# Performance work log

Hardware: AMD Instinct MI355X
Metric: run time of the kernel (lower is better)

Reference implementation:

```python
import jax, jax.numpy as jnp
import numpy as np

N_HEADS = 16
NOPE = 128
ROPE = 64
VDIM = 128
HEAD_DIM = NOPE + ROPE  # 192


def apply_rope(x, cos, sin):
    # x: [B, S, H, D] with D even; pairs (a, b) rotated by complex freqs.
    B, S, H, D = x.shape
    xr = x.reshape(B, S, H, D // 2, 2)
    a, b = xr[..., 0], xr[..., 1]
    c = cos[None, :, None, :]
    s = sin[None, :, None, :]
    out = jnp.stack([a * c - b * s, a * s + b * c], axis=-1)
    return out.reshape(B, S, H, D)


def setup_inputs() -> dict:
    key = jax.random.key(0)
    ks = jax.random.split(key, 8)
    B, S, DIM = 1, 2048, 2048
    x = jax.random.normal(ks[0], (B, S, DIM), dtype=jnp.float32)
    wq = jax.random.normal(ks[1], (N_HEADS * HEAD_DIM, DIM), dtype=jnp.float32) * (DIM ** -0.5)
    wk = jax.random.normal(ks[2], (N_HEADS * HEAD_DIM, DIM), dtype=jnp.float32) * (DIM ** -0.5)
    wv = jax.random.normal(ks[3], (N_HEADS * VDIM, DIM), dtype=jnp.float32) * (DIM ** -0.5)
    wo = jax.random.normal(ks[4], (DIM, N_HEADS * VDIM), dtype=jnp.float32) * ((N_HEADS * VDIM) ** -0.5)
    # rotary freqs: theta = 10000^{-2i/d}, angles = pos * theta
    inv_freq = 1.0 / (10000.0 ** (np.arange(0, ROPE, 2, dtype=np.float32) / ROPE))
    angles = np.arange(S, dtype=np.float32)[:, None] * inv_freq[None, :]  # [S, 32]
    freqs_cos = jnp.asarray(np.cos(angles))
    freqs_sin = jnp.asarray(np.sin(angles))
    # additive causal mask
    mask = jnp.where(jnp.triu(jnp.ones((S, S), dtype=bool), k=1), -1e9, 0.0).astype(jnp.float32)
    return {"x": x, "wq": wq, "wk": wk, "wv": wv, "wo": wo,
            "freqs_cos": freqs_cos, "freqs_sin": freqs_sin, "mask": mask, "start_pos": 0}


def reference(x, wq, wk, wv, wo, freqs_cos, freqs_sin, mask, start_pos):
    B, S, DIM = x.shape
    q = (x @ wq.T).reshape(B, S, N_HEADS, HEAD_DIM)
    k = (x @ wk.T).reshape(B, S, N_HEADS, HEAD_DIM)
    v = (x @ wv.T).reshape(B, S, N_HEADS, VDIM)
    q_nope, q_pe = q[..., :NOPE], q[..., NOPE:]
    k_nope, k_pe = k[..., :NOPE], k[..., NOPE:]
    q_pe = apply_rope(q_pe, freqs_cos, freqs_sin)
    k_pe = apply_rope(k_pe, freqs_cos, freqs_sin)
    scores = (jnp.einsum('bshd,bthd->bsht', q_nope, k_nope)
              + jnp.einsum('bshd,bthd->bsht', q_pe, k_pe)) * (HEAD_DIM ** -0.5)
    scores = scores + mask[None, :, None, :]
    probs = jax.nn.softmax(scores.astype(jnp.float32), axis=-1).astype(x.dtype)
    out = jnp.einsum('bsht,bthd->bshd', probs, v)
    return out.reshape(B, S, N_HEADS * VDIM) @ wo.T
```

## Files before the change

### kernel.cpp

```cpp
#include <hip/hip_runtime.h>
#include <hip/hip_bf16.h>
#include <math.h>

#define NH 16
#define NOPE 128
#define ROPE 64
#define VDIM 128
#define HD 192
#define SEQ 2048
#define DIM 2048
#define QKD (NH * HD)
#define VD  (NH * VDIM)
#define QKVS 8192

typedef __attribute__((ext_vector_type(8))) short short8;
typedef __attribute__((ext_vector_type(4))) short short4v;
typedef __attribute__((ext_vector_type(4))) float f32x4;
typedef unsigned int u32;

#define WAIT_VM8  0x0F78
#define WAIT_VM6  0x0F76
#define WAIT_VM4  0x0F74
#define WAIT_VM0  0x0F70
#define WAIT_LGKM 0xC07F

static __device__ inline short f2bf(float f) {
  union { float f; unsigned u; } v; v.f = f;
  unsigned r = (v.u + 0x7fffu + ((v.u >> 16) & 1u)) >> 16;
  return (short)r;
}
static __device__ inline float bf2f(unsigned short u) {
  union { unsigned u; float f; } v; v.u = ((unsigned)u) << 16;
  return v.f;
}

static __device__ __forceinline__ void gload16(const short* g, short* l) {
  __builtin_amdgcn_global_load_lds(
      (const __attribute__((address_space(1))) u32*)g,
      (__attribute__((address_space(3))) u32*)l, 16, 0, 0);
}


#define LSA(pp) (Lsm + (pp) * 65536)
#define LSB(pp) (Lsm + (pp) * 65536 + 32768)

#define RDA(pp, kh, mh) do { \
  const char* p_ = LSA(pp) + abase + (mh) * 8192 + ((kh) ? cx1 : cx0); \
  afr[(mh) * 4 + 0] = *(const short8*)(p_ + 0); \
  afr[(mh) * 4 + 1] = *(const short8*)(p_ + 2048); \
  afr[(mh) * 4 + 2] = *(const short8*)(p_ + 4096); \
  afr[(mh) * 4 + 3] = *(const short8*)(p_ + 6144); \
} while (0)

#define RDB(pp, kh) do { \
  const char* p_ = LSB(pp) + bbase + ((kh) ? cx1 : cx0); \
  bfr[0] = *(const short8*)(p_ + 0); \
  bfr[1] = *(const short8*)(p_ + 2048); \
  bfr[2] = *(const short8*)(p_ + 4096); \
  bfr[3] = *(const short8*)(p_ + 6144); \
} while (0)

#define SGA(kt, c) gload16(srcA[c] + (kt) * 64, (short*)(LSA((kt) & 1) + ((c) * 512 + tid) * 16))
#define SGB(kt, c) gload16(srcB[c] + (kt) * 64, (short*)(LSB((kt) & 1) + ((c) * 512 + tid) * 16))
#define G1S(kt) do { SGA(kt, 0); SGA(kt, 2); SGB(kt, 0); SGB(kt, 1); } while (0)
#define G2S(kt) do { SGA(kt, 1); SGA(kt, 3); SGB(kt, 2); SGB(kt, 3); } while (0)

#define MFMA1(mi, ni) \
  acc[mi][ni] = __builtin_amdgcn_mfma_f32_16x16x32_bf16(afr[mi], bfr[ni], acc[mi][ni], 0, 0, 0)

#define MM(mh) do { \
  MFMA1((mh)*4+0, 0); MFMA1((mh)*4+1, 0); MFMA1((mh)*4+2, 0); MFMA1((mh)*4+3, 0); \
  MFMA1((mh)*4+0, 1); MFMA1((mh)*4+1, 1); MFMA1((mh)*4+2, 1); MFMA1((mh)*4+3, 1); \
  MFMA1((mh)*4+0, 2); MFMA1((mh)*4+1, 2); MFMA1((mh)*4+2, 2); MFMA1((mh)*4+3, 2); \
  MFMA1((mh)*4+0, 3); MFMA1((mh)*4+1, 3); MFMA1((mh)*4+2, 3); MFMA1((mh)*4+3, 3); \
} while (0)

#define GBAR() __builtin_amdgcn_s_barrier()
#define GLGKM0() __builtin_amdgcn_s_waitcnt(WAIT_LGKM)
#define GPRIO1() __builtin_amdgcn_s_setprio(1)
#define GPRIO0() __builtin_amdgcn_s_setprio(0)
#define GNOP ((void)0)

#define TILE(pp, SP1, SP4, VMW) do { \
  RDA(pp, 0, 0); RDB(pp, 0); SP1; \
  GBAR(); GLGKM0(); GPRIO1(); MM(0); GPRIO0(); GBAR(); \
  RDA(pp, 0, 1); \
  GBAR(); GLGKM0(); GPRIO1(); MM(1); GPRIO0(); GBAR(); \
  RDA(pp, 1, 0); RDB(pp, 1); \
  GBAR(); GLGKM0(); GPRIO1(); MM(0); GPRIO0(); GBAR(); \
  RDA(pp, 1, 1); SP4; \
  GBAR(); GLGKM0(); GPRIO1(); MM(1); GPRIO0(); VMW; GBAR(); \
} while (0)

__global__ __launch_bounds__(512, 2) void gemm256_bt(
    const short* __restrict__ A, const short* __restrict__ B,
    short* __restrict__ C, int K, int lda, int ldb, int ldc) {
  __shared__ __align__(16) char Lsm[131072];

  const int tid = threadIdx.x;
  const int lane = tid & 63;
  const int l15 = lane & 15;
  const int quad = lane >> 4;
  const int wv = tid >> 6;
  const int wr = wv >> 2, wc = wv & 3;

  const int bid = blockIdx.x;
  const int xcd = bid & 7;
  const int idx = bid >> 3;
  const int m0 = (idx & 7) * 256;
  const int n0 = (xcd * 4 + (idx >> 3)) * 256;

  const int trow = tid >> 3;
  const int scol = ((tid & 7) * 8) ^ ((trow & 7) * 8);
  const short* srcA[4]; const short* srcB[4];
#pragma unroll
  for (int c = 0; c < 4; ++c) {
    srcA[c] = A + (size_t)(m0 + c * 64 + trow) * lda + scol;
    srcB[c] = B + (size_t)(n0 + c * 64 + trow) * ldb + scol;
  }

  const int abase = (wr * 128 + l15) * 128;
  const int bbase = (wc * 64 + l15) * 128;
  const int cx0 = (quad * 16) ^ ((l15 & 7) * 16);
  const int cx1 = (64 + quad * 16) ^ ((l15 & 7) * 16);

  f32x4 acc[8][4];
#pragma unroll
  for (int i = 0; i < 8; ++i)
#pragma unroll
    for (int j = 0; j < 4; ++j) acc[i][j] = (f32x4)(0.f);
  short8 afr[8], bfr[4];

  const int NT = K >> 6;

  G1S(0); G2S(0); G1S(1);
  __builtin_amdgcn_s_waitcnt(WAIT_VM4);
  GBAR();

  int kt = 0;
  for (; kt + 4 <= NT; kt += 2) {
    TILE(0, G2S(kt + 1), G1S(kt + 2), __builtin_amdgcn_s_waitcnt(WAIT_VM4));
    TILE(1, G2S(kt + 2), G1S(kt + 3), __builtin_amdgcn_s_waitcnt(WAIT_VM4));
  }
  TILE(0, G2S(kt + 1), GNOP, __builtin_amdgcn_s_waitcnt(WAIT_VM0));
  TILE(1, GNOP, GNOP, GNOP);

#pragma unroll
  for (int m = 0; m < 8; ++m) {
    const size_t rb = (size_t)(m0 + wr * 128 + m * 16 + quad * 4) * ldc +
                      n0 + wc * 64 + l15;
#pragma unroll
    for (int n = 0; n < 4; ++n)
#pragma unroll
      for (int r = 0; r < 4; ++r)
        C[rb + (size_t)r * ldc + n * 16] = f2bf(acc[m][n][r]);
  }
}

template <bool BF16OUT>
__global__ __launch_bounds__(256) void gemm_bt(
    const short* __restrict__ A, const short* __restrict__ B,
    void* __restrict__ Cv, int K, int lda, int ldb, int ldc, float oscale) {
  __shared__ __align__(16) short Ls[4][2][4096];

  const int tid = threadIdx.x;
  const int lane = tid & 63;
  const int wave = tid >> 6;
  const int wr = wave >> 1, wc = wave & 1;
  const int lane15 = lane & 15, quad = lane >> 4;
  const int m0 = blockIdx.y * 128, n0 = blockIdx.x * 128;

  const short* gA[4]; const short* gB[4];
#pragma unroll
  for (int i = 0; i < 4; ++i) {
    int gidx = i * 64 + lane;
    int r = gidx >> 2, p = gidx & 3;
    int g = (p ^ ((r >> 1) & 3)) * 8;
    gA[i] = A + (size_t)(m0 + wr * 64 + r) * lda + g;
    gB[i] = B + (size_t)(n0 + wc * 64 + r) * ldb + g;
  }

  f32x4 acc[4][4];
#pragma unroll
  for (int i = 0; i < 4; ++i)
#pragma unroll
    for (int j = 0; j < 4; ++j) acc[i][j] = (f32x4)(0.f);

#pragma unroll
  for (int i = 0; i < 4; ++i) gload16(gA[i], &Ls[wave][0][i * 512]);
#pragma unroll
  for (int i = 0; i < 4; ++i) gload16(gB[i], &Ls[wave][0][2048 + i * 512]);

  const int rsw = (lane15 >> 1) & 3;
  for (int k0 = 0; k0 < K; k0 += 32) {
    const int cur = (k0 >> 5) & 1;
    __builtin_amdgcn_s_waitcnt(WAIT_LGKM);
    if (k0 + 32 < K) {
      const int nxt = cur ^ 1;
#pragma unroll
      for (int i = 0; i < 4; ++i) gload16(gA[i] + k0 + 32, &Ls[wave][nxt][i * 512]);
#pragma unroll
      for (int i = 0; i < 4; ++i) gload16(gB[i] + k0 + 32, &Ls[wave][nxt][2048 + i * 512]);
      __builtin_amdgcn_s_waitcnt(WAIT_VM8);
    } else {
      __builtin_amdgcn_s_waitcnt(WAIT_VM0);
    }
    const short* bufp = &Ls[wave][cur][0];
    short8 af[4], bfv[4];
#pragma unroll
    for (int i = 0; i < 4; ++i)
      af[i] = *(const short8*)&bufp[(i * 16 + lane15) * 32 + (quad ^ rsw) * 8];
#pragma unroll
    for (int j = 0; j < 4; ++j)
      bfv[j] = *(const short8*)&bufp[2048 + (j * 16 + lane15) * 32 + (quad ^ rsw) * 8];
#pragma unroll
    for (int i = 0; i < 4; ++i)
#pragma unroll
      for (int j = 0; j < 4; ++j)
        acc[i][j] = __builtin_amdgcn_mfma_f32_16x16x32_bf16(af[i], bfv[j], acc[i][j], 0, 0, 0);
  }

#pragma unroll
  for (int i = 0; i < 4; ++i)
#pragma unroll
    for (int j = 0; j < 4; ++j)
#pragma unroll
      for (int r = 0; r < 4; ++r) {
        size_t idx = (size_t)(m0 + wr * 64 + i * 16 + quad * 4 + r) * ldc +
                     n0 + wc * 64 + j * 16 + lane15;
        if (BF16OUT)
          ((short*)Cv)[idx] = f2bf(acc[i][j][r] * oscale);
        else
          ((float*)Cv)[idx] = acc[i][j][r];
      }
}

__global__ __launch_bounds__(256) void rope_qk(
    short* __restrict__ qk, const float* __restrict__ cosf, const float* __restrict__ sinf) {
  int idx = blockIdx.x * blockDim.x + threadIdx.x;
  int j = idx & 31;
  int h = (idx >> 5) & (NH - 1);
  int s = idx >> 9;
  if (s >= SEQ) return;

  float c = cosf[s * 32 + j];
  float sn = sinf[s * 32 + j];
  size_t rowb = (size_t)s * QKVS + h * HD + NOPE + 2 * j;

  u32* pq = (u32*)(qk + rowb);
  u32 w = *pq;
  float a = bf2f((unsigned short)(w & 0xffff));
  float b = bf2f((unsigned short)(w >> 16));
  *pq = (u32)(unsigned short)f2bf(a * c - b * sn) |
        ((u32)(unsigned short)f2bf(a * sn + b * c) << 16);

  u32* pk = (u32*)(qk + rowb + QKD);
  w = *pk;
  a = bf2f((unsigned short)(w & 0xffff));
  b = bf2f((unsigned short)(w >> 16));
  *pk = (u32)(unsigned short)f2bf(a * c - b * sn) |
        ((u32)(unsigned short)f2bf(a * sn + b * c) << 16);
}

__global__ __launch_bounds__(256) void bf16_convert(
    const float* __restrict__ in, short* __restrict__ out, int n4) {
  int i = blockIdx.x * 256 + threadIdx.x;
  if (i >= n4) return;
  float4 f = ((const float4*)in)[i];
  short4v o;
  o.x = f2bf(f.x); o.y = f2bf(f.y); o.z = f2bf(f.z); o.w = f2bf(f.w);
  ((short4v*)out)[i] = o;
}

__global__ __launch_bounds__(256) void conv_wqkv(
    const float* __restrict__ wq, const float* __restrict__ wk,
    const float* __restrict__ wv, short* __restrict__ wqkv, int n4) {
  int i = blockIdx.x * 256 + threadIdx.x;
  if (i >= n4) return;
  int row = i >> 9;
  float4 f;
  if (row < QKD) f = ((const float4*)wq)[i];
  else if (row < 2 * QKD) f = ((const float4*)wk)[i - QKD * (DIM / 4)];
  else f = ((const float4*)wv)[i - 2 * QKD * (DIM / 4)];
  short4v o;
  o.x = f2bf(f.x); o.y = f2bf(f.y); o.z = f2bf(f.z); o.w = f2bf(f.w);
  ((short4v*)wqkv)[i] = o;
}

__global__ __launch_bounds__(256) void vt_bf16(
    const short* __restrict__ vb, short* __restrict__ vtb) {
  __shared__ short tile[64][74];
  const int t0 = blockIdx.x * 64;
  const int c0 = blockIdx.y * 64;
  const int tid = threadIdx.x;
#pragma unroll
  for (int i = 0; i < 16; ++i) {
    int idx = i * 256 + tid;
    int r = idx >> 6, c = idx & 63;
    tile[r][c] = vb[(size_t)(t0 + r) * QKVS + c0 + c];
  }
  __syncthreads();
  const int h = c0 >> 7;
  const int dbase = c0 & 127;
#pragma unroll
  for (int i = 0; i < 16; ++i) {
    int idx = i * 256 + tid;
    int d = idx >> 6, t = idx & 63;
    vtb[(size_t)h * VDIM * SEQ + (size_t)(dbase + d) * SEQ + t0 + t] = tile[t][d];
  }
}

#define BQ 128
#define BT 64
#define CHT 8
#define PSTR 76
#define MFIX 8.0f

__global__ __launch_bounds__(512, 4) void attn_part(
    const short* __restrict__ qk,
    const short* __restrict__ vtb,
    short* __restrict__ Opart,
    float* __restrict__ lpart)
{
  __shared__ __align__(16) short Ks[BT * 192];
  __shared__ __align__(16) short Vt[VDIM * BT];
  __shared__ __align__(16) short Ps[8 * 16 * PSTR];

  const int xcd = blockIdx.x;
  const int i0 = blockIdx.y;
  const int h = xcd + ((i0 >= 40) ? 8 : 0);
  int jj = (i0 >= 40) ? (i0 - 40) : i0;
  int qtb = 15;
  while (jj >= (qtb >> 2) + 1) { jj -= (qtb >> 2) + 1; --qtb; }
  const int chk = jj;

  const int tid = threadIdx.x;
  const int wave = tid >> 6;
  const int lane = tid & 63;
  const int lane15 = lane & 15;
  const int quad = lane >> 4;
  const int g = qtb >> 2;
  const int slot = h * 40 + (g + 1) * (2 * g + (qtb & 3)) + chk;
  const int R0 = qtb * BQ;
  const int NT = 2 * qtb + 2;
  const int kt_beg = chk * CHT;
  const int kt_end = min(kt_beg + CHT, NT);
  const float scale = 0.072168784f;

  const int qrow = R0 + wave * 16 + lane15;
  short8 qf[6];
  const short* qbase = qk + (size_t)qrow * QKVS + h * HD + quad * 8;
#pragma unroll
  for (int kc = 0; kc < 6; ++kc) qf[kc] = *(const short8*)(qbase + kc * 32);

  const short* kb = qk + QKD;
  int lKoff[3]; const short* gK[3];
#pragma unroll
  for (int i = 0; i < 3; ++i) {
    int id = i * 512 + tid;
    int row = id / 24, cX = id - row * 24;
    int ch = cX ^ (row & 7);
    lKoff[i] = id * 8;
    gK[i] = kb + (size_t)row * QKVS + h * HD + ch * 8;
  }
  const short* gV[2]; short* lV[2];
#pragma unroll
  for (int i = 0; i < 2; ++i) {
    int id = i * 512 + tid;
    int row = id >> 3, cX = id & 7;
    int ch = cX ^ (row & 7);
    lV[i] = &Vt[id * 8];
    gV[i] = vtb + (size_t)h * VDIM * SEQ + (size_t)row * SEQ + ch * 8;
  }

  f32x4 oacc[8];
#pragma unroll
  for (int i = 0; i < 8; ++i) oacc[i] = (f32x4)(0.f);
  float lsum[4] = {0.f, 0.f, 0.f, 0.f};

  short* pw = &Ps[wave * 16 * PSTR];

  for (int kt = kt_beg; kt < kt_end; ++kt) {
    const int t0 = kt * BT;
    __syncthreads();
#pragma unroll
    for (int i = 0; i < 3; ++i) gload16(gK[i] + (size_t)t0 * QKVS, &Ks[lKoff[i]]);
#pragma unroll
    for (int i = 0; i < 2; ++i) gload16(gV[i] + t0, lV[i]);
    __syncthreads();

    f32x4 sacc[4];
    __builtin_amdgcn_s_setprio(1);
#pragma unroll
    for (int c = 0; c < 4; ++c) {
      sacc[c] = (f32x4)(0.f);
      const int row = c * 16 + lane15;
#pragma unroll
      for (int kc = 0; kc < 6; ++kc) {
        int cX = (4 * kc + quad) ^ (lane15 & 7);
        short8 kf = *(const short8*)&Ks[row * 192 + cX * 8];
        sacc[c] = __builtin_amdgcn_mfma_f32_16x16x32_bf16(qf[kc], kf, sacc[c], 0, 0, 0);
      }
    }
    __builtin_amdgcn_s_setprio(0);

    if (kt >= 2 * qtb) {
#pragma unroll
      for (int c = 0; c < 4; ++c)
#pragma unroll
        for (int r = 0; r < 4; ++r) {
          int tg = t0 + c * 16 + lane15;
          int qg = R0 + wave * 16 + quad * 4 + r;
          if (tg > qg) sacc[c][r] = -1e30f;
        }
    }

#pragma unroll
    for (int c = 0; c < 4; ++c)
#pragma unroll
      for (int r = 0; r < 4; ++r) {
        float p = __expf(sacc[c][r] * scale - MFIX);
        lsum[r] += p;
        pw[(quad * 4 + r) * PSTR + c * 16 + lane15] = f2bf(p);
      }

    short8 pf0 = *(const short8*)&pw[lane15 * PSTR + quad * 8];
    short8 pf1 = *(const short8*)&pw[lane15 * PSTR + 32 + quad * 8];
    __builtin_amdgcn_s_setprio(1);
#pragma unroll
    for (int ch = 0; ch < 8; ++ch) {
      const int row = ch * 16 + lane15;
      int cX0 = quad ^ (lane15 & 7);
      int cX1 = (4 + quad) ^ (lane15 & 7);
      short8 vf0 = *(const short8*)&Vt[row * 64 + cX0 * 8];
      short8 vf1 = *(const short8*)&Vt[row * 64 + cX1 * 8];
      oacc[ch] = __builtin_amdgcn_mfma_f32_16x16x32_bf16(pf0, vf0, oacc[ch], 0, 0, 0);
      oacc[ch] = __builtin_amdgcn_mfma_f32_16x16x32_bf16(pf1, vf1, oacc[ch], 0, 0, 0);
    }
    __builtin_amdgcn_s_setprio(0);
  }

  short* op = Opart + (size_t)slot * (128 * 128);
#pragma unroll
  for (int ch = 0; ch < 8; ++ch)
#pragma unroll
    for (int r = 0; r < 4; ++r)
      op[(wave * 16 + quad * 4 + r) * 128 + ch * 16 + lane15] = f2bf(oacc[ch][r]);

  float red[4];
#pragma unroll
  for (int r = 0; r < 4; ++r) {
    float s = lsum[r];
    s += __shfl_xor(s, 1, 64);
    s += __shfl_xor(s, 2, 64);
    s += __shfl_xor(s, 4, 64);
    s += __shfl_xor(s, 8, 64);
    red[r] = s;
  }
  if (lane15 == 0) {
#pragma unroll
    for (int r = 0; r < 4; ++r)
      lpart[(size_t)slot * 128 + wave * 16 + quad * 4 + r] = red[r];
  }
}

__global__ __launch_bounds__(256) void attn_combine(
    const short* __restrict__ Opart, const float* __restrict__ lpart,
    short* __restrict__ aob) {
  const int qt64 = blockIdx.x, h = blockIdx.y;
  const int qtb = qt64 >> 1;
  const int half = qt64 & 1;
  const int g = qtb >> 2;
  const int nact = g + 1;
  const int base = h * 40 + (g + 1) * (2 * g + (qtb & 3));
  const int tid = threadIdx.x;
  const int row = tid >> 2;
  const int cg = (tid & 3) * 32;

  float acc[32];
#pragma unroll
  for (int e = 0; e < 32; ++e) acc[e] = 0.f;
  float lsum = 0.f;

  for (int c = 0; c < nact; ++c) {
    const short* sp = Opart + (size_t)(base + c) * (128 * 128) +
                      (half * 64 + row) * 128 + cg;
    lsum += lpart[(size_t)(base + c) * 128 + half * 64 + row];
#pragma unroll
    for (int gg = 0; gg < 4; ++gg) {
      short8 vv = *(const short8*)(sp + gg * 8);
#pragma unroll
      for (int e = 0; e < 8; ++e) acc[gg * 8 + e] += bf2f((unsigned short)vv[e]);
    }
  }

  float inv = 1.f / lsum;
#pragma unroll
  for (int gg = 0; gg < 4; ++gg) {
    short8 ov;
#pragma unroll
    for (int e = 0; e < 8; ++e) ov[e] = f2bf(acc[gg * 8 + e] * inv);
    *(short8*)(aob + (size_t)(qt64 * 64 + row) * VD + h * 128 + cg + gg * 8) = ov;
  }
}

extern "C" void kernel_launch(void* const* d_in, const int* in_sizes, int n_in,
                              void* d_out, int out_size, void* d_ws, size_t ws_size,
                              hipStream_t stream) {
  const float* x  = (const float*)d_in[0];
  const float* wq = (const float*)d_in[1];
  const float* wk = (const float*)d_in[2];
  const float* wv = (const float*)d_in[3];
  const float* wo = (const float*)d_in[4];
  const float* fc = (const float*)d_in[5];
  const float* fs = (const float*)d_in[6];

  char* ws8 = (char*)d_ws;
  short* xb    = (short*)(ws8 + 0);
  short* wo_b  = (short*)(ws8 + 0);
  short* wqkv  = (short*)(ws8 + 8388608);
  short* vtb   = (short*)(ws8 + 8388608);
  short* Opart = (short*)(ws8 + 16777216);
  float* lpart = (float*)(ws8 + 37748736);
  short* qkv   = (short*)(ws8 + 41943040);
  short* aob   = qkv;
  float* out   = (float*)d_out;

  const int NX4 = DIM * DIM / 4;
  const int NQKV4 = QKVS * DIM / 4;
  const int ROPE_GRID = (SEQ * NH * 32) / 256;

  bf16_convert<<<(NX4 + 255) / 256, 256, 0, stream>>>(x, xb, NX4);
  conv_wqkv<<<(NQKV4 + 255) / 256, 256, 0, stream>>>(wq, wk, wv, wqkv, NQKV4);

  gemm256_bt<<<dim3((QKVS / 256) * (SEQ / 256)), 512, 0, stream>>>(
      xb, wqkv, qkv, DIM, DIM, DIM, QKVS);
  rope_qk<<<ROPE_GRID, 256, 0, stream>>>(qkv, fc, fs);
  vt_bf16<<<dim3(SEQ / 64, VD / 64), 256, 0, stream>>>(qkv + 2 * QKD, vtb);

  bf16_convert<<<(NX4 + 255) / 256, 256, 0, stream>>>(wo, wo_b, NX4);

  attn_part<<<dim3(8, 80), 512, 0, stream>>>(qkv, vtb, Opart, lpart);
  attn_combine<<<dim3(SEQ / 64, NH), 256, 0, stream>>>(Opart, lpart, aob);

  gemm_bt<false><<<dim3(DIM / 128, SEQ / 128), 256, 0, stream>>>(
      aob, wo_b, out, DIM, VD, DIM, DIM, 1.0f);
}
```

Measured before the change: 312.7 us.

## Double-buffer K tiles in attention and fuse input conversion kernels

The attention kernel now double-buffers the K tile in shared memory, prefetching the next tile during the current QK^T and PV MFMAs. V is still single-buffered and reloaded after PV, with explicit waitcnt and barrier instructions replacing __syncthreads. The P staging buffer is halved by writing and consuming P in two 32-column halves. The x and wqkv fp32-to-bf16 conversions are merged into one launch to save a kernel launch. The extra K buffer raises LDS use per block, which may hurt occupancy, and the V reload still serializes part of each iteration.

After: 312.2 us. About the same (-0.1%).

```diff
diff --git a/kernel.cpp b/kernel.cpp
--- a/kernel.cpp
+++ b/kernel.cpp
@@ -21,6 +21,8 @@
 #define WAIT_VM8  0x0F78
 #define WAIT_VM6  0x0F76
 #define WAIT_VM4  0x0F74
+#define WAIT_VM3  0x0F73
+#define WAIT_VM2  0x0F72
 #define WAIT_VM0  0x0F70
 #define WAIT_LGKM 0xC07F
 
@@ -262,6 +264,28 @@
         ((u32)(unsigned short)f2bf(a * sn + b * c) << 16);
 }
 
+__global__ __launch_bounds__(256) void conv_in(
+    const float* __restrict__ x, const float* __restrict__ wq,
+    const float* __restrict__ wk, const float* __restrict__ wv,
+    short* __restrict__ xb, short* __restrict__ wqkv) {
+  const int NX4v = DIM * DIM / 4;
+  int i = blockIdx.x * 256 + threadIdx.x;
+  float4 f; short* dst; int di;
+  if (i < NX4v) {
+    f = ((const float4*)x)[i]; dst = xb; di = i;
+  } else {
+    int j = i - NX4v;
+    int row = j >> 9;
+    if (row < QKD) f = ((const float4*)wq)[j];
+    else if (row < 2 * QKD) f = ((const float4*)wk)[j - QKD * (DIM / 4)];
+    else f = ((const float4*)wv)[j - 2 * QKD * (DIM / 4)];
+    dst = wqkv; di = j;
+  }
+  short4v o;
+  o.x = f2bf(f.x); o.y = f2bf(f.y); o.z = f2bf(f.z); o.w = f2bf(f.w);
+  ((short4v*)dst)[di] = o;
+}
+
 __global__ __launch_bounds__(256) void bf16_convert(
     const float* __restrict__ in, short* __restrict__ out, int n4) {
   int i = blockIdx.x * 256 + threadIdx.x;
@@ -272,21 +296,6 @@
   ((short4v*)out)[i] = o;
 }
 
-__global__ __launch_bounds__(256) void conv_wqkv(
-    const float* __restrict__ wq, const float* __restrict__ wk,
-    const float* __restrict__ wv, short* __restrict__ wqkv, int n4) {
-  int i = blockIdx.x * 256 + threadIdx.x;
-  if (i >= n4) return;
-  int row = i >> 9;
-  float4 f;
-  if (row < QKD) f = ((const float4*)wq)[i];
-  else if (row < 2 * QKD) f = ((const float4*)wk)[i - QKD * (DIM / 4)];
-  else f = ((const float4*)wv)[i - 2 * QKD * (DIM / 4)];
-  short4v o;
-  o.x = f2bf(f.x); o.y = f2bf(f.y); o.z = f2bf(f.z); o.w = f2bf(f.w);
-  ((short4v*)wqkv)[i] = o;
-}
-
 __global__ __launch_bounds__(256) void vt_bf16(
     const short* __restrict__ vb, short* __restrict__ vtb) {
   __shared__ short tile[64][74];
@@ -313,7 +322,7 @@
 #define BQ 128
 #define BT 64
 #define CHT 8
-#define PSTR 76
+#define PSTR2 36
 #define MFIX 8.0f
 
 __global__ __launch_bounds__(512, 4) void attn_part(
@@ -322,9 +331,9 @@
     short* __restrict__ Opart,
     float* __restrict__ lpart)
 {
-  __shared__ __align__(16) short Ks[BT * 192];
+  __shared__ __align__(16) short Ks[2][BT * 192];
   __shared__ __align__(16) short Vt[VDIM * BT];
-  __shared__ __align__(16) short Ps[8 * 16 * PSTR];
+  __shared__ __align__(16) short Ps[8 * 16 * PSTR2];
 
   const int xcd = blockIdx.x;
   const int i0 = blockIdx.y;
@@ -352,6 +361,8 @@
   const short* qbase = qk + (size_t)qrow * QKVS + h * HD + quad * 8;
 #pragma unroll
   for (int kc = 0; kc < 6; ++kc) qf[kc] = *(const short8*)(qbase + kc * 32);
+  __builtin_amdgcn_s_waitcnt(WAIT_VM0);
+  __builtin_amdgcn_sched_barrier(0);
 
   const short* kb = qk + QKD;
   int lKoff[3]; const short* gK[3];
@@ -378,17 +389,30 @@
   for (int i = 0; i < 8; ++i) oacc[i] = (f32x4)(0.f);
   float lsum[4] = {0.f, 0.f, 0.f, 0.f};
 
-  short* pw = &Ps[wave * 16 * PSTR];
+  short* pw = &Ps[wave * 16 * PSTR2];
+
+  {
+    const size_t t0 = (size_t)kt_beg * BT;
+#pragma unroll
+    for (int i = 0; i < 3; ++i) gload16(gK[i] + t0 * QKVS, &Ks[0][lKoff[i]]);
+#pragma unroll
+    for (int i = 0; i < 2; ++i) gload16(gV[i] + t0, lV[i]);
+  }
+  __builtin_amdgcn_s_waitcnt(WAIT_VM2);
+  __builtin_amdgcn_s_barrier();
+  __builtin_amdgcn_sched_barrier(0);
 
   for (int kt = kt_beg; kt < kt_end; ++kt) {
-    const int t0 = kt * BT;
-    __syncthreads();
-#pragma unroll
-    for (int i = 0; i < 3; ++i) gload16(gK[i] + (size_t)t0 * QKVS, &Ks[lKoff[i]]);
-#pragma unroll
-    for (int i = 0; i < 2; ++i) gload16(gV[i] + t0, lV[i]);
-    __syncthreads();
-
+    const int cur = (kt - kt_beg) & 1;
+    const bool have = (kt + 1 < kt_end);
+
+    if (have) {
+      const size_t tn = (size_t)(kt + 1) * BT;
+#pragma unroll
+      for (int i = 0; i < 3; ++i) gload16(gK[i] + tn * QKVS, &Ks[cur ^ 1][lKoff[i]]);
+    }
+
+    const short* kcur = &Ks[cur][0];
     f32x4 sacc[4];
     __builtin_amdgcn_s_setprio(1);
 #pragma unroll
@@ -398,7 +422,7 @@
 #pragma unroll
       for (int kc = 0; kc < 6; ++kc) {
         int cX = (4 * kc + quad) ^ (lane15 & 7);
-        short8 kf = *(const short8*)&Ks[row * 192 + cX * 8];
+        short8 kf = *(const short8*)&kcur[row * 192 + cX * 8];
         sacc[c] = __builtin_amdgcn_mfma_f32_16x16x32_bf16(qf[kc], kf, sacc[c], 0, 0, 0);
       }
     }
@@ -409,7 +433,7 @@
       for (int c = 0; c < 4; ++c)
 #pragma unroll
         for (int r = 0; r < 4; ++r) {
-          int tg = t0 + c * 16 + lane15;
+          int tg = kt * BT + c * 16 + lane15;
           int qg = R0 + wave * 16 + quad * 4 + r;
           if (tg > qg) sacc[c][r] = -1e30f;
         }
@@ -421,23 +445,57 @@
       for (int r = 0; r < 4; ++r) {
         float p = __expf(sacc[c][r] * scale - MFIX);
         lsum[r] += p;
-        pw[(quad * 4 + r) * PSTR + c * 16 + lane15] = f2bf(p);
+        sacc[c][r] = p;
       }
 
-    short8 pf0 = *(const short8*)&pw[lane15 * PSTR + quad * 8];
-    short8 pf1 = *(const short8*)&pw[lane15 * PSTR + 32 + quad * 8];
+#pragma unroll
+    for (int c = 0; c < 2; ++c)
+#pragma unroll
+      for (int r = 0; r < 4; ++r)
+        pw[(quad * 4 + r) * PSTR2 + c * 16 + lane15] = f2bf(sacc[c][r]);
+    short8 pf0 = *(const short8*)&pw[lane15 * PSTR2 + quad * 8];
+
+    if (have) __builtin_amdgcn_s_waitcnt(WAIT_VM3);
+    else      __builtin_amdgcn_s_waitcnt(WAIT_VM0);
+    __builtin_amdgcn_s_barrier();
+    __builtin_amdgcn_sched_barrier(0);
+
     __builtin_amdgcn_s_setprio(1);
 #pragma unroll
     for (int ch = 0; ch < 8; ++ch) {
       const int row = ch * 16 + lane15;
       int cX0 = quad ^ (lane15 & 7);
+      short8 vf0 = *(const short8*)&Vt[row * 64 + cX0 * 8];
+      oacc[ch] = __builtin_amdgcn_mfma_f32_16x16x32_bf16(pf0, vf0, oacc[ch], 0, 0, 0);
+    }
+    __builtin_amdgcn_s_setprio(0);
+
+#pragma unroll
+    for (int c = 0; c < 2; ++c)
+#pragma unroll
+      for (int r = 0; r < 4; ++r)
+        pw[(quad * 4 + r) * PSTR2 + c * 16 + lane15] = f2bf(sacc[2 + c][r]);
+    short8 pf1 = *(const short8*)&pw[lane15 * PSTR2 + quad * 8];
+    __builtin_amdgcn_s_setprio(1);
+#pragma unroll
+    for (int ch = 0; ch < 8; ++ch) {
+      const int row = ch * 16 + lane15;
       int cX1 = (4 + quad) ^ (lane15 & 7);
-      short8 vf0 = *(const short8*)&Vt[row * 64 + cX0 * 8];
       short8 vf1 = *(const short8*)&Vt[row * 64 + cX1 * 8];
-      oacc[ch] = __builtin_amdgcn_mfma_f32_16x16x32_bf16(pf0, vf0, oacc[ch], 0, 0, 0);
       oacc[ch] = __builtin_amdgcn_mfma_f32_16x16x32_bf16(pf1, vf1, oacc[ch], 0, 0, 0);
     }
     __builtin_amdgcn_s_setprio(0);
+
+    if (have) {
+      __builtin_amdgcn_s_waitcnt(WAIT_LGKM);
+      __builtin_amdgcn_s_barrier();
+      const size_t tn = (size_t)(kt + 1) * BT;
+#pragma unroll
+      for (int i = 0; i < 2; ++i) gload16(gV[i] + tn, lV[i]);
+      __builtin_amdgcn_s_waitcnt(WAIT_VM2);
+      __builtin_amdgcn_s_barrier();
+      __builtin_amdgcn_sched_barrier(0);
+    }
   }
 
   short* op = Opart + (size_t)slot * (128 * 128);
@@ -530,8 +588,7 @@
   const int NQKV4 = QKVS * DIM / 4;
   const int ROPE_GRID = (SEQ * NH * 32) / 256;
 
-  bf16_convert<<<(NX4 + 255) / 256, 256, 0, stream>>>(x, xb, NX4);
-  conv_wqkv<<<(NQKV4 + 255) / 256, 256, 0, stream>>>(wq, wk, wv, wqkv, NQKV4);
+  conv_in<<<(NX4 + NQKV4) / 256, 256, 0, stream>>>(x, wq, wk, wv, xb, wqkv);
 
   gemm256_bt<<<dim3((QKVS / 256) * (SEQ / 256)), 512, 0, stream>>>(
       xb, wqkv, qkv, DIM, DIM, DIM, QKVS);
```
